# Performance work log

Hardware: AMD Instinct MI355X
Metric: run time of the kernel (lower is better)

The kernel has to match this reference:

```python
import jax, jax.numpy as jnp
import numpy as np

FEATURE_DIM = 512
NUM_HEADS = 8
HEAD_DIM = FEATURE_DIM // NUM_HEADS


def setup_inputs() -> dict:
    key = jax.random.key(0)
    ks = jax.random.split(key, 16)
    B, N, F = 16, 768, FEATURE_DIM
    Nb = N // 3
    s = 1.0 / np.sqrt(F)
    inp = {
        "x_1": jax.random.normal(ks[0], (B, N, F), jnp.float32),
        "x_2": jax.random.normal(ks[1], (B, N, F), jnp.float32),
        "z_b": jax.random.normal(ks[2], (Nb, F), jnp.float32),
        # weights stored [in, out] (torch Linear applies x @ W.T)
        "Wqkv_i": jax.random.normal(ks[3], (F, 3 * F), jnp.float32) * s,
        "Wqkv_j": jax.random.normal(ks[4], (F, 3 * F), jnp.float32) * s,
        "Wqkv_b": jax.random.normal(ks[5], (F, 3 * F), jnp.float32) * s,
        "W_f": jax.random.normal(ks[6], (2 * F, F), jnp.float32) * s,
        "b_f": jnp.zeros((F,), jnp.float32),
        "W_m": jax.random.normal(ks[7], (F, F), jnp.float32) * s,
        "b_m": jnp.zeros((F,), jnp.float32),
        "W_QKV": jax.random.normal(ks[8], (F, 3 * F), jnp.float32) * s,
        "W_proj": jax.random.normal(ks[9], (F, F), jnp.float32) * s,
        "b_proj": jnp.zeros((F,), jnp.float32),
    }
    return inp


def reference(x_1, x_2, z_b, Wqkv_i, Wqkv_j, Wqkv_b, W_f, b_f, W_m, b_m, W_QKV, W_proj, b_proj):
    z_i, z_j = x_1, x_2
    B, N, F = z_i.shape
    Nb = z_b.shape[0]
    scale = F ** -0.5           # full-dim attention scale
    Scale = HEAD_DIM ** -0.5    # multi-head attention scale

    zb = jnp.broadcast_to((z_b * 0.2)[None], (B, Nb, F))

    def split_qkv(x, W):
        qkv = (x @ W).reshape(x.shape[0], x.shape[1], 3, F)
        return qkv[:, :, 0], qkv[:, :, 1], qkv[:, :, 2]

    _, k_i, v_i = split_qkv(z_i, Wqkv_i)
    q_j, _, _ = split_qkv(z_j, Wqkv_j)
    q_b, k_b, v_b = split_qkv(zb, Wqkv_b)

    # bottleneck cross attentions (single-head, full feature dim)
    a_ib = jax.nn.softmax(jnp.einsum('bmf,bnf->bmn', q_b, k_i) * scale, axis=-1)  # [B,Nb,N]
    a_bj = jax.nn.softmax(jnp.einsum('bnf,bmf->bnm', q_j, k_b) * scale, axis=-1)  # [B,N,Nb]

    a_ib = jnp.einsum('bmn,bnf->bmf', a_ib, v_i)  # [B,Nb,F]
    attn_up = jax.nn.softmax(jnp.einsum('bnf,bmf->bnm', z_i, a_ib) * scale, axis=-1)  # [B,N,Nb]
    a_ib = jnp.einsum('bnm,bmf->bnf', attn_up, a_ib)  # [B,N,F]
    a_bj = jnp.einsum('bnm,bmf->bnf', a_bj, v_b)      # [B,N,F]
    a_ij = (a_ib + a_bj) * 0.5

    # gated fusion
    f_ij = jax.nn.sigmoid(jnp.concatenate([a_ij, z_j], axis=-1) @ W_f + b_f)
    h_ij = jax.nn.relu(z_i + (a_ij @ W_m + b_m) * f_ij)

    # standard multi-head self-attention
    QKV = (h_ij @ W_QKV).reshape(B, N, 3, NUM_HEADS, HEAD_DIM)
    Q, K, V = [jnp.transpose(QKV[:, :, t], (0, 2, 1, 3)) for t in range(3)]  # [B,H,N,hd]
    Attn = jax.nn.softmax(jnp.einsum('bhnd,bhmd->bhnm', Q, K) * Scale, axis=-1)
    H = jnp.einsum('bhnm,bhmd->bhnd', Attn, V)
    H = jnp.transpose(H, (0, 2, 1, 3)).reshape(B, N, F)
    return H @ W_proj + b_proj
```

## Files before the change

kernel.cpp:

```cpp
#include <hip/hip_runtime.h>
#include <hip/hip_bf16.h>

typedef __attribute__((ext_vector_type(8))) short short8;
typedef __attribute__((ext_vector_type(4))) float f32x4;
typedef __hip_bfloat16 bf16;
typedef unsigned short ushort;

__device__ __forceinline__ ushort f2b(float v) {
    bf16 h = __float2bfloat16(v);
    return *reinterpret_cast<ushort*>(&h);
}
__device__ __forceinline__ float b2f(ushort u) {
    return __uint_as_float((unsigned)u << 16);
}

#define GLD16(lds, gp) __builtin_amdgcn_global_load_lds( \
    (const __attribute__((address_space(1))) void*)(gp), \
    (__attribute__((address_space(3))) void*)(lds), 16, 0, 0)

template<typename OutT, int EPI, int TM>
__global__ __launch_bounds__(256) void gemm_bf16(
    const bf16* __restrict__ A, const bf16* __restrict__ B, OutT* __restrict__ C,
    int K, int lda, int ldb, int ldc, long sA, long sB, long sC,
    float alpha, const float* __restrict__ bias,
    const float* __restrict__ e1, const float* __restrict__ e2, int eld, long sE,
    bf16* __restrict__ px, bf16* __restrict__ py)
{
    constexpr int RT = TM / 32;
    constexpr int AHW = TM * 32;
    constexpr int BHW = 128 * 32;
    __shared__ __align__(16) bf16 As[2 * AHW];
    __shared__ __align__(16) bf16 Bs[2 * BHW];

    const int t = threadIdx.x;
    const int w = t >> 6, lane = t & 63;
    const int wr = w >> 1, wc = w & 1;
    const int lr = lane & 15, kc4 = lane >> 4;
    const int qr = lane >> 2;
    const int kcr = ((lane & 3) - ((lane >> 3) & 3)) & 3;
    const int row0 = blockIdx.y * TM, col0 = blockIdx.x * 128;
    const int bz = blockIdx.z;

    const bf16* Asel = A; const bf16* Bsel = B;
    int abz = bz; long sBe = sB; int ldbe = ldb;
    if constexpr (EPI == 7) {
        if (bz >= 16) {
            Asel = (const bf16*)px; Bsel = (const bf16*)py;
            abz = bz - 16; sBe = 0; ldbe = eld;
        }
    }
    const bf16* Ab = Asel + (size_t)abz * sA + (size_t)row0 * lda;
    const bf16* Bb = Bsel + (size_t)abz * sBe + (size_t)col0 * ldbe;

    const bf16* ga0; const bf16* ga1 = nullptr;
    if constexpr (TM == 64) {
        ga0 = Ab + (size_t)(w * 16 + qr) * lda + kcr * 8;
    } else {
        ga0 = Ab + (size_t)(w * 32 + qr) * lda + kcr * 8;
        ga1 = Ab + (size_t)(w * 32 + 16 + qr) * lda + kcr * 8;
    }
    const bf16* gb0 = Bb + (size_t)(w * 32 + qr) * ldbe + kcr * 8;
    const bf16* gb1 = Bb + (size_t)(w * 32 + 16 + qr) * ldbe + kcr * 8;
    bf16* lA0; bf16* lA1 = nullptr;
    if constexpr (TM == 64) { lA0 = &As[w * 512]; }
    else                    { lA0 = &As[w * 1024]; lA1 = &As[w * 1024 + 512]; }
    bf16* lB0 = &Bs[w * 1024];
    bf16* lB1 = &Bs[w * 1024 + 512];

    f32x4 acc[RT][4] = {};

    const int cSw = ((kc4 + ((lr >> 1) & 3)) & 3) * 8;
    const bf16* ApBase = &As[(wr * (TM / 2) + lr) * 32 + cSw];
    const bf16* BpBase = &Bs[(wc * 64 + lr) * 32 + cSw];

    GLD16(lA0, ga0);
    if constexpr (TM == 128) GLD16(lA1, ga1);
    GLD16(lB0, gb0); GLD16(lB1, gb1);

    auto step = [&](int kk, int rd, int st) {
        __syncthreads();
        const int kn = kk + 32;
        if (kn < K) {
            GLD16(lA0 + st * AHW, ga0 + kn);
            if constexpr (TM == 128) GLD16(lA1 + st * AHW, ga1 + kn);
            GLD16(lB0 + st * BHW, gb0 + kn);
            GLD16(lB1 + st * BHW, gb1 + kn);
        }
        const bf16* Ap = ApBase + rd * AHW;
        const bf16* Bp = BpBase + rd * BHW;
        short8 af[RT], bfr[4];
#pragma unroll
        for (int i = 0; i < RT; ++i) af[i]  = *(const short8*)(Ap + i * 512);
#pragma unroll
        for (int j = 0; j < 4; ++j) bfr[j] = *(const short8*)(Bp + j * 512);
#pragma unroll
        for (int i = 0; i < RT; ++i)
#pragma unroll
            for (int j = 0; j < 4; ++j)
                acc[i][j] = __builtin_amdgcn_mfma_f32_16x16x32_bf16(af[i], bfr[j], acc[i][j], 0, 0, 0);
    };

    for (int k0 = 0; k0 < K; k0 += 64) {
        step(k0, 0, 1);
        step(k0 + 32, 1, 0);
    }

    if constexpr (EPI == 4) {
        const int sec = blockIdx.x >> 2;
        const int h0 = (blockIdx.x & 3) * 2;
        const int b  = blockIdx.y / 6;
        const int n0 = (blockIdx.y % 6) * TM;
        bf16* dq = (bf16*)C;
#pragma unroll
        for (int j = 0; j < 4; ++j) {
            const int col = wc * 64 + j * 16 + lr;
            const int h = h0 + (col >> 6), hd = col & 63;
            const size_t bh = (size_t)b * 8 + h;
#pragma unroll
            for (int i = 0; i < RT; ++i) {
                const int n = n0 + wr * (TM / 2) + i * 16 + kc4 * 4;
                if (sec == 2) {
                    __align__(8) ushort o[4];
#pragma unroll
                    for (int r = 0; r < 4; ++r) o[r] = f2b(acc[i][j][r]);
                    *(int2*)&py[(bh * 64 + hd) * 768 + n] = *(const int2*)o;
                } else {
                    bf16* d = (sec == 0) ? dq : px;
#pragma unroll
                    for (int r = 0; r < 4; ++r)
                        d[(bh * 768 + n + r) * 64 + hd] = __float2bfloat16(acc[i][j][r]);
                }
            }
        }
        return;
    } else if constexpr (EPI == 5) {
        const int b  = blockIdx.y / 6;
        const int n0 = (blockIdx.y % 6) * TM;
#pragma unroll
        for (int j = 0; j < 4; ++j) {
            const int col = col0 + wc * 64 + j * 16 + lr;
#pragma unroll
            for (int i = 0; i < RT; ++i) {
                const int n = n0 + wr * (TM / 2) + i * 16 + kc4 * 4;
                if (col < 512) {
#pragma unroll
                    for (int r = 0; r < 4; ++r)
                        ((bf16*)C)[((size_t)b * 768 + n + r) * 512 + col] = __float2bfloat16(acc[i][j][r]);
                } else {
                    __align__(8) ushort o[4];
#pragma unroll
                    for (int r = 0; r < 4; ++r) o[r] = f2b(acc[i][j][r]);
                    *(int2*)&py[((size_t)b * 512 + (col - 512)) * 768 + n] = *(const int2*)o;
                }
            }
        }
        return;
    }

    OutT* Cb = C + (size_t)bz * sC;
#pragma unroll
    for (int j = 0; j < 4; ++j) {
        const int col = col0 + wc * 64 + j * 16 + lr;
        const float bv = bias ? bias[col] : 0.f;
#pragma unroll
        for (int i = 0; i < RT; ++i) {
            const int rb = row0 + wr * (TM / 2) + i * 16 + kc4 * 4;
            if constexpr (EPI == 6) {
                __align__(8) ushort o[4];
#pragma unroll
                for (int r = 0; r < 4; ++r) {
                    o[r] = f2b(alpha * acc[i][j][r]);
                    Cb[(size_t)(rb + r) * ldc + col] = __float2bfloat16(alpha * acc[i][j][r]);
                }
                *(int2*)&py[(size_t)bz * sE + (size_t)col * eld + rb] = *(const int2*)o;
            } else {
#pragma unroll
                for (int r = 0; r < 4; ++r) {
                    const int row = rb + r;
                    float v = alpha * acc[i][j][r] + bv;
                    if constexpr (sizeof(OutT) == 2)
                        Cb[(size_t)row * ldc + col] = __float2bfloat16(v);
                    else
                        Cb[(size_t)row * ldc + col] = v;
                }
            }
        }
    }
}

__global__ __launch_bounds__(256) void gemm_gate(
    const bf16* __restrict__ A, const bf16* __restrict__ Bf,
    const bf16* __restrict__ Bm, bf16* __restrict__ Cout,
    const float* __restrict__ bias_f, const float* __restrict__ bias_m,
    const float* __restrict__ x1)
{
    constexpr int AHW = 64 * 32;
    constexpr int BHW = 128 * 32;
    __shared__ __align__(16) bf16 As[2 * AHW];
    __shared__ __align__(16) bf16 FsS[2 * BHW];
    __shared__ __align__(16) bf16 MsS[2 * BHW];

    const int t = threadIdx.x;
    const int w = t >> 6, lane = t & 63;
    const int wr = w >> 1, wc = w & 1;
    const int lr = lane & 15, kc4 = lane >> 4;
    const int qr = lane >> 2;
    const int kcr = ((lane & 3) - ((lane >> 3) & 3)) & 3;
    const int row0 = blockIdx.y * 64, col0 = blockIdx.x * 128;

    const bf16* ga0 = A  + (size_t)(row0 + w * 16 + qr) * 1024 + kcr * 8;
    const bf16* gf0 = Bf + (size_t)(col0 + w * 32 + qr) * 1024 + kcr * 8;
    const bf16* gf1 = Bf + (size_t)(col0 + w * 32 + 16 + qr) * 1024 + kcr * 8;
    const bf16* gm0 = Bm + (size_t)(col0 + w * 32 + qr) * 512 + kcr * 8;
    const bf16* gm1 = Bm + (size_t)(col0 + w * 32 + 16 + qr) * 512 + kcr * 8;
    bf16* lA0 = &As[w * 512];
    bf16* lF0 = &FsS[w * 1024]; bf16* lF1 = &FsS[w * 1024 + 512];
    bf16* lM0 = &MsS[w * 1024]; bf16* lM1 = &MsS[w * 1024 + 512];

    f32x4 acc1[2][4] = {};
    f32x4 acc2[2][4] = {};

    const int cSw = ((kc4 + ((lr >> 1) & 3)) & 3) * 8;
    const bf16* ApBase = &As[(wr * 32 + lr) * 32 + cSw];
    const bf16* FpBase = &FsS[(wc * 64 + lr) * 32 + cSw];
    const bf16* MpBase = &MsS[(wc * 64 + lr) * 32 + cSw];

    GLD16(lA0, ga0);
    GLD16(lF0, gf0); GLD16(lF1, gf1);
    GLD16(lM0, gm0); GLD16(lM1, gm1);

    auto step = [&](int kk, int rd, int st) {
        __syncthreads();
        const int kn = kk + 32;
        if (kn < 1024) {
            GLD16(lA0 + st * AHW, ga0 + kn);
            GLD16(lF0 + st * BHW, gf0 + kn);
            GLD16(lF1 + st * BHW, gf1 + kn);
            if (kn < 512) {
                GLD16(lM0 + st * BHW, gm0 + kn);
                GLD16(lM1 + st * BHW, gm1 + kn);
            }
        }
        const bf16* Ap = ApBase + rd * AHW;
        const bf16* Fp = FpBase + rd * BHW;
        short8 af[2], ff[4];
#pragma unroll
        for (int i = 0; i < 2; ++i) af[i] = *(const short8*)(Ap + i * 512);
#pragma unroll
        for (int j = 0; j < 4; ++j) ff[j] = *(const short8*)(Fp + j * 512);
#pragma unroll
        for (int i = 0; i < 2; ++i)
#pragma unroll
            for (int j = 0; j < 4; ++j)
                acc1[i][j] = __builtin_amdgcn_mfma_f32_16x16x32_bf16(af[i], ff[j], acc1[i][j], 0, 0, 0);
        if (kk < 512) {
            const bf16* Mp = MpBase + rd * BHW;
            short8 mf[4];
#pragma unroll
            for (int j = 0; j < 4; ++j) mf[j] = *(const short8*)(Mp + j * 512);
#pragma unroll
            for (int i = 0; i < 2; ++i)
#pragma unroll
                for (int j = 0; j < 4; ++j)
                    acc2[i][j] = __builtin_amdgcn_mfma_f32_16x16x32_bf16(af[i], mf[j], acc2[i][j], 0, 0, 0);
        }
    };

    for (int k0 = 0; k0 < 1024; k0 += 64) {
        step(k0, 0, 1);
        step(k0 + 32, 1, 0);
    }

#pragma unroll
    for (int j = 0; j < 4; ++j) {
        const int col = col0 + wc * 64 + j * 16 + lr;
        const float bvf = bias_f[col], bvm = bias_m[col];
#pragma unroll
        for (int i = 0; i < 2; ++i) {
            const int rb = row0 + wr * 32 + i * 16 + kc4 * 4;
#pragma unroll
            for (int r = 0; r < 4; ++r) {
                const int row = rb + r;
                const float sig = 1.f / (1.f + __expf(-(acc1[i][j][r] + bvf)));
                const float rr = x1[(size_t)row * 512 + col] + (acc2[i][j][r] + bvm) * sig;
                Cout[(size_t)row * 512 + col] = __float2bfloat16(rr > 0.f ? rr : 0.f);
            }
        }
    }
}

template<typename TI, int NSRC>
__global__ __launch_bounds__(256) void k_transpose(
    const TI* __restrict__ s0, const TI* __restrict__ s1,
    const TI* __restrict__ s2, const TI* __restrict__ s3,
    bf16* __restrict__ dst, int src_ld, int dst_ld, long sSrc, long sDst,
    int rep, long repStride)
{
    __shared__ float tile[64][65];
    const int t = threadIdx.x;
    const int c0 = blockIdx.x * 64, r0 = blockIdx.y * 64;
    const int z = blockIdx.z;
    const TI* src = s0;
    if (NSRC > 1) src = (z == 0) ? s0 : (z == 1) ? s1 : (z == 2) ? s2 : s3;
    {
        const int r = t >> 2, cq = (t & 3) * 16;
        const TI* sp = src + (size_t)z * sSrc + (size_t)(r0 + r) * src_ld + c0 + cq;
        if constexpr (sizeof(TI) == 4) {
#pragma unroll
            for (int u = 0; u < 16; u += 4) {
                float4 v = *(const float4*)((const float*)sp + u);
                tile[r][cq + u]     = v.x; tile[r][cq + u + 1] = v.y;
                tile[r][cq + u + 2] = v.z; tile[r][cq + u + 3] = v.w;
            }
        } else {
            const ushort* up = (const ushort*)sp;
            union { short8 v; ushort u[8]; } p0, p1;
            p0.v = *(const short8*)up; p1.v = *(const short8*)(up + 8);
#pragma unroll
            for (int u = 0; u < 8; ++u) {
                tile[r][cq + u]     = b2f(p0.u[u]);
                tile[r][cq + 8 + u] = b2f(p1.u[u]);
            }
        }
    }
    __syncthreads();
    const int c = t >> 2, rq = (t & 3) * 16;
    __align__(16) ushort ob[16];
#pragma unroll
    for (int u = 0; u < 16; ++u) ob[u] = f2b(tile[rq + u][c]);
    for (int rp = 0; rp < rep; ++rp) {
        bf16* dp = dst + (size_t)rp * repStride + (size_t)z * sDst + (size_t)(c0 + c) * dst_ld + r0 + rq;
        *(int4*)dp       = *(const int4*)&ob[0];
        *(int4*)(dp + 8) = *(const int4*)&ob[8];
    }
}

__global__ __launch_bounds__(256) void k_cast3(const float* __restrict__ x1,
    const float* __restrict__ x2, const float* __restrict__ zb,
    bf16* __restrict__ d1, bf16* __restrict__ d2, bf16* __restrict__ d3)
{
    const int z = blockIdx.z;
    const float* src; bf16* dst; int ld; float scale; int n;
    if (z == 0)      { src = x1; dst = d1; ld = 512;  scale = 1.f;  n = 6291456; }
    else if (z == 1) { src = x2; dst = d2; ld = 1024; scale = 1.f;  n = 6291456; }
    else             { src = zb; dst = d3; ld = 512;  scale = 0.2f; n = 131072;  }
    int i = (blockIdx.x * 256 + threadIdx.x) * 8;
    if (i >= n) return;
    float4 a = *(const float4*)(src + i), b = *(const float4*)(src + i + 4);
    __align__(16) ushort o[8];
    o[0] = f2b(a.x * scale); o[1] = f2b(a.y * scale); o[2] = f2b(a.z * scale); o[3] = f2b(a.w * scale);
    o[4] = f2b(b.x * scale); o[5] = f2b(b.y * scale); o[6] = f2b(b.z * scale); o[7] = f2b(b.w * scale);
    int row = i >> 9, col = i & 511;
    *(int4*)(dst + (size_t)row * ld + col) = *(const int4*)o;
}

template<int COLS, int MODE>
__global__ __launch_bounds__(256) void softmax_wave(const float* __restrict__ X,
                                                    bf16* __restrict__ Y)
{
    const int wv = threadIdx.x >> 6, lane = threadIdx.x & 63;
    const long row = (long)blockIdx.x * 4 + wv;
    const float* src = X + row * COLS;
    constexpr int V = COLS / 64;
    float v[V];
#pragma unroll
    for (int i = 0; i < V; ++i) v[i] = src[lane + i * 64];
    float m = v[0];
#pragma unroll
    for (int i = 1; i < V; ++i) m = fmaxf(m, v[i]);
#pragma unroll
    for (int o = 32; o; o >>= 1) m = fmaxf(m, __shfl_xor(m, o));
    float s = 0.f;
#pragma unroll
    for (int i = 0; i < V; ++i) { v[i] = __expf(v[i] - m); s += v[i]; }
#pragma unroll
    for (int o = 32; o; o >>= 1) s += __shfl_xor(s, o);
    const float inv = 1.f / s;
    bf16* dst;
    if constexpr (MODE == 0) {
        dst = Y + row * COLS;
    } else {
        const int z = (int)(row / 768), mm = (int)(row % 768);
        dst = Y + ((size_t)(z & 15) * 768 + mm) * 512 + (z >> 4) * 256;
    }
#pragma unroll
    for (int i = 0; i < V; ++i) dst[lane + i * 64] = __float2bfloat16(v[i] * inv);
}

__global__ __launch_bounds__(256) void mhsa_flash_mfma(
    const bf16* __restrict__ Qb, const bf16* __restrict__ Kb,
    const bf16* __restrict__ VT, bf16* __restrict__ Hout)
{
    constexpr int LD = 72;
    __shared__ __align__(16) ushort Qs[64 * LD];
    __shared__ __align__(16) ushort Ks[64 * LD];
    __shared__ __align__(16) ushort Vt[64 * LD];
    __shared__ __align__(16) ushort Ps[64 * LD];

    const int t = threadIdx.x;
    const int w = t >> 6, lane = t & 63;
    const int l16 = lane & 15, q4 = lane >> 4;
    const int h = blockIdx.x, b = blockIdx.y, qt = blockIdx.z;
    const size_t bh = (size_t)b * 8 + h;
    const ushort* qbase = (const ushort*)Qb + bh * 768 * 64;
    const ushort* kbase = (const ushort*)Kb + bh * 768 * 64;
    const ushort* vbase = (const ushort*)VT + bh * 64 * 768;

    const int r = t >> 2, c0 = (t & 3) * 16;

    {
        const ushort* src = qbase + (size_t)(qt * 64 + r) * 64 + c0;
        *(int4*)&Qs[r * LD + c0]     = *(const int4*)src;
        *(int4*)&Qs[r * LD + c0 + 8] = *(const int4*)(src + 8);
    }

    int4 ka0, ka1, va0, va1;
    {
        const ushort* ks = kbase + (size_t)r * 64 + c0;
        ka0 = *(const int4*)ks; ka1 = *(const int4*)(ks + 8);
        const ushort* vs = vbase + (size_t)r * 768 + c0;
        va0 = *(const int4*)vs; va1 = *(const int4*)(vs + 8);
    }
    __syncthreads();

    short8 qf0 = *(const short8*)&Qs[(w * 16 + l16) * LD + q4 * 8];
    short8 qf1 = *(const short8*)&Qs[(w * 16 + l16) * LD + 32 + q4 * 8];

    float lsum[4] = {0.f, 0.f, 0.f, 0.f};
    f32x4 acc[4] = {};

    for (int kt = 0; kt < 12; ++kt) {
        if (kt) __syncthreads();
        *(int4*)&Ks[r * LD + c0]     = ka0;
        *(int4*)&Ks[r * LD + c0 + 8] = ka1;
        *(int4*)&Vt[r * LD + c0]     = va0;
        *(int4*)&Vt[r * LD + c0 + 8] = va1;
        __syncthreads();

        if (kt < 11) {
            const ushort* ks = kbase + (size_t)((kt + 1) * 64 + r) * 64 + c0;
            ka0 = *(const int4*)ks; ka1 = *(const int4*)(ks + 8);
            const ushort* vs = vbase + (size_t)r * 768 + (kt + 1) * 64 + c0;
            va0 = *(const int4*)vs; va1 = *(const int4*)(vs + 8);
        }

        f32x4 s[4] = {};
#pragma unroll
        for (int nt = 0; nt < 4; ++nt) {
            short8 kf0 = *(const short8*)&Ks[(nt * 16 + l16) * LD + q4 * 8];
            short8 kf1 = *(const short8*)&Ks[(nt * 16 + l16) * LD + 32 + q4 * 8];
            s[nt] = __builtin_amdgcn_mfma_f32_16x16x32_bf16(qf0, kf0, s[nt], 0, 0, 0);
            s[nt] = __builtin_amdgcn_mfma_f32_16x16x32_bf16(qf1, kf1, s[nt], 0, 0, 0);
        }

#pragma unroll
        for (int nt = 0; nt < 4; ++nt) {
#pragma unroll
            for (int e = 0; e < 4; ++e) {
                const float p = __expf(s[nt][e] * 0.125f);
                lsum[e] += p;
                Ps[(w * 16 + q4 * 4 + e) * LD + nt * 16 + l16] = f2b(p);
            }
        }

        short8 pf0 = *(const short8*)&Ps[(w * 16 + l16) * LD + q4 * 8];
        short8 pf1 = *(const short8*)&Ps[(w * 16 + l16) * LD + 32 + q4 * 8];
#pragma unroll
        for (int jt = 0; jt < 4; ++jt) {
            short8 vf0 = *(const short8*)&Vt[(jt * 16 + l16) * LD + q4 * 8];
            short8 vf1 = *(const short8*)&Vt[(jt * 16 + l16) * LD + 32 + q4 * 8];
            acc[jt] = __builtin_amdgcn_mfma_f32_16x16x32_bf16(pf0, vf0, acc[jt], 0, 0, 0);
            acc[jt] = __builtin_amdgcn_mfma_f32_16x16x32_bf16(pf1, vf1, acc[jt], 0, 0, 0);
        }
    }

    const int orow = qt * 64 + w * 16 + q4 * 4;
#pragma unroll
    for (int e = 0; e < 4; ++e) {
        float l = lsum[e];
        l += __shfl_xor(l, 1);
        l += __shfl_xor(l, 2);
        l += __shfl_xor(l, 4);
        l += __shfl_xor(l, 8);
        const float inv = 1.f / l;
        const size_t rbase = ((size_t)b * 768 + orow + e) * 512 + h * 64;
#pragma unroll
        for (int jt = 0; jt < 4; ++jt)
            Hout[rbase + jt * 16 + l16] = __float2bfloat16(acc[jt][e] * inv);
    }
}

extern "C" void kernel_launch(void* const* d_in, const int* in_sizes, int n_in,
                              void* d_out, int out_size, void* d_ws, size_t ws_size,
                              hipStream_t stream)
{
    (void)in_sizes; (void)n_in; (void)out_size; (void)ws_size;
    const float* x1     = (const float*)d_in[0];
    const float* x2     = (const float*)d_in[1];
    const float* z_b    = (const float*)d_in[2];
    const float* Wqkv_i = (const float*)d_in[3];
    const float* Wqkv_j = (const float*)d_in[4];
    const float* Wqkv_b = (const float*)d_in[5];
    const float* W_f    = (const float*)d_in[6];
    const float* b_f    = (const float*)d_in[7];
    const float* W_m    = (const float*)d_in[8];
    const float* b_m    = (const float*)d_in[9];
    const float* W_QKV  = (const float*)d_in[10];
    const float* W_proj = (const float*)d_in[11];
    const float* b_proj = (const float*)d_in[12];
    float* out = (float*)d_out;

    const float scale = 0.044194173824159216f;

    char* base = (char*)d_ws;
    size_t off = 0;
    auto alloc = [&](size_t bytes) { char* r = base + off; off += (bytes + 255) & ~(size_t)255; return r; };

    char* Rq  = alloc((size_t)3 * 25165824);
    char* R1  = Rq;
    char* R2  = Rq + 25165824;
    char* R3  = Rq + 2 * 25165824;
    char* R4  = alloc(25165824);
    bf16* Wt4     = (bf16*)alloc((size_t)4 * 1536 * 512 * 2);
    bf16* Wt_f    = (bf16*)alloc(512 * 1024 * 2);
    bf16* Wt_mp   = (bf16*)alloc((size_t)2 * 512 * 512 * 2);
    bf16* c_zb    = (bf16*)alloc(256 * 512 * 2);
    bf16* qkvb    = (bf16*)alloc(256 * 1536 * 2);
    bf16* aib0    = (bf16*)alloc((size_t)16 * 256 * 512 * 2);
    bf16* Bcat    = (bf16*)alloc((size_t)16 * 512 * 512 * 2);
    float* S      = (float*)alloc((size_t)32 * 768 * 256 * 4);
    bf16* Sb1     = (bf16*)alloc((size_t)16 * 256 * 768 * 2);
    bf16* Sb_cat  = (bf16*)alloc((size_t)16 * 768 * 512 * 2);
    bf16* c_cat   = (bf16*)alloc((size_t)12288 * 1024 * 2);
    bf16* hbuf    = (bf16*)alloc((size_t)12288 * 512 * 2);

    bf16* Wt_i = Wt4, *Wt_j = Wt4 + 1536 * 512, *Wt_b = Wt4 + 2 * 1536 * 512,
        *Wt_qkv = Wt4 + (size_t)3 * 1536 * 512;
    bf16* Wt_m = Wt_mp, *Wt_proj = Wt_mp + 512 * 512;

    bf16*  Kc   = (bf16*)R1;
    bf16*  Qb   = (bf16*)R1;
    bf16*  Kb   = (bf16*)(R1 + 12582912);
    bf16*  v_iT = (bf16*)R2;
    bf16*  VTb  = (bf16*)R2;
    bf16*  c_x1 = (bf16*)R3;
    bf16*  qj   = (bf16*)R4;   bf16* Hout = (bf16*)R4;

    auto G64 = [&](const bf16* A, const bf16* B, void* C, bool outBf,
                   int M, int N, int K, int lda, int ldb, int ldc,
                   long sA, long sB, long sC, int batch, float alpha, const float* bias) {
        dim3 grid(N / 128, M / 64, batch);
        if (outBf) gemm_bf16<bf16, 0, 64><<<grid, 256, 0, stream>>>(A, B, (bf16*)C, K, lda, ldb, ldc, sA, sB, sC, alpha, bias, nullptr, nullptr, 0, 0, nullptr, nullptr);
        else       gemm_bf16<float, 0, 64><<<grid, 256, 0, stream>>>(A, B, (float*)C, K, lda, ldb, ldc, sA, sB, sC, alpha, bias, nullptr, nullptr, 0, 0, nullptr, nullptr);
    };

    k_cast3<<<dim3(3072, 1, 3), 256, 0, stream>>>(x1, x2, z_b, c_x1, c_cat + 512, c_zb);
    k_transpose<float, 4><<<dim3(24, 8, 4), 256, 0, stream>>>(
        Wqkv_i, Wqkv_j, Wqkv_b, W_QKV, Wt4, 1536, 512, 0, 1536L * 512, 1, 0);
    k_transpose<float, 1><<<dim3(8, 16, 1), 256, 0, stream>>>(
        W_f, nullptr, nullptr, nullptr, Wt_f, 512, 1024, 0, 0, 1, 0);
    k_transpose<float, 2><<<dim3(8, 8, 2), 256, 0, stream>>>(
        W_m, W_proj, nullptr, nullptr, Wt_mp, 512, 512, 0, 512L * 512, 1, 0);

    G64(c_zb, Wt_b, qkvb, true, 256, 1536, 512, 512, 512, 1536, 0, 0, 0, 1, 1.f, nullptr);
    k_transpose<bf16, 1><<<dim3(8, 4, 1), 256, 0, stream>>>(
        qkvb + 1024, nullptr, nullptr, nullptr, Bcat + 256, 1536, 512, 0, 0, 16, 512L * 512);
    gemm_bf16<bf16, 5, 128><<<dim3(8, 96, 1), 256, 0, stream>>>(
        c_x1, Wt_i + 512 * 512, Kc, 512, 512, 512, 512, 0, 0, 0,
        1.f, nullptr, nullptr, nullptr, 0, 0, nullptr, v_iT);
    G64(c_cat + 512, Wt_j, qj, true, 12288, 512, 512, 1024, 512, 512, 0, 0, 0, 1, 1.f, nullptr);
    G64(qkvb, Kc, S, false, 256, 768, 512, 1536, 512, 768, 0, 768L * 512, 256L * 768, 16, scale, nullptr);
    softmax_wave<768, 0><<<1024, 256, 0, stream>>>(S, Sb1);
    gemm_bf16<bf16, 6, 64><<<dim3(4, 4, 16), 256, 0, stream>>>(
        Sb1, v_iT, aib0, 768, 768, 768, 512, 256L * 768, 512L * 768, 256L * 512,
        1.f, nullptr, nullptr, nullptr, 512, 512L * 512, nullptr, Bcat);
    gemm_bf16<float, 7, 64><<<dim3(2, 12, 32), 256, 0, stream>>>(
        c_x1, aib0, S, 512, 512, 512, 256, 768L * 512, 256L * 512, 768L * 256,
        scale, nullptr, nullptr, nullptr, 1536, 0, qj, qkvb + 512);
    softmax_wave<256, 1><<<6144, 256, 0, stream>>>(S, Sb_cat);
    G64(Sb_cat, Bcat, c_cat, true, 768, 512, 512, 512, 512, 1024,
        768L * 512, 512L * 512, 768L * 1024, 16, 0.5f, nullptr);
    gemm_gate<<<dim3(4, 192), 256, 0, stream>>>(c_cat, Wt_f, Wt_m, hbuf, b_f, b_m, x1);
    gemm_bf16<bf16, 4, 128><<<dim3(12, 96, 1), 256, 0, stream>>>(
        hbuf, Wt_qkv, Qb, 512, 512, 512, 0, 0, 0, 0,
        1.f, nullptr, nullptr, nullptr, 0, 0, Kb, VTb);
    mhsa_flash_mfma<<<dim3(8, 16, 12), 256, 0, stream>>>(Qb, Kb, VTb, Hout);
    G64(Hout, Wt_proj, out, false, 12288, 512, 512, 512, 512, 512, 0, 0, 0, 1, 1.f, b_proj);
}
```

Measured before the change: 401.6 us.

## Fold q_j projection into k_b, swizzle GEMM blocks across XCDs, deepen pipeline

Computes q_j·k_b^T as x_2·(Wq_j·k_b^T) by first forming a small G = k_b·Wq_j^T matrix, which removes the 12288x512x512 q_j projection GEMM. The EPI 7 GEMM gains separate lda/stride arguments so it can read x_2 directly from c_cat. Separately, 2D GEMM grids get an XCD-aware block remap for L2 locality. The TM=64 GEMM path now prefetches two 32-wide K planes per barrier, using double the LDS, while the TM=128 path gets a simpler single-plane loop. These bring more LDS use and extra small launches, and change the order of rounding for the bf16 products.

```diff
diff --git a/kernel.cpp b/kernel.cpp
--- a/kernel.cpp
+++ b/kernel.cpp
@@ -17,20 +17,30 @@
 #define GLD16(lds, gp) __builtin_amdgcn_global_load_lds( \
     (const __attribute__((address_space(1))) void*)(gp), \
     (__attribute__((address_space(3))) void*)(lds), 16, 0, 0)
+
+__device__ __forceinline__ void xcd_swizzle(int& bx, int& by) {
+    if (gridDim.z == 1 && (gridDim.y & 7) == 0) {
+        const int id = bx + gridDim.x * by;
+        const int xcd = id & 7, slot = id >> 3;
+        by = xcd * (gridDim.y >> 3) + slot / gridDim.x;
+        bx = slot - (slot / gridDim.x) * gridDim.x;
+    }
+}
 
 template<typename OutT, int EPI, int TM>
 __global__ __launch_bounds__(256) void gemm_bf16(
     const bf16* __restrict__ A, const bf16* __restrict__ B, OutT* __restrict__ C,
     int K, int lda, int ldb, int ldc, long sA, long sB, long sC,
     float alpha, const float* __restrict__ bias,
-    const float* __restrict__ e1, const float* __restrict__ e2, int eld, long sE,
+    int lda2, long sA2, int eld, long sE,
     bf16* __restrict__ px, bf16* __restrict__ py)
 {
     constexpr int RT = TM / 32;
-    constexpr int AHW = TM * 32;
-    constexpr int BHW = 128 * 32;
-    __shared__ __align__(16) bf16 As[2 * AHW];
-    __shared__ __align__(16) bf16 Bs[2 * BHW];
+    constexpr int PLA = TM * 32;
+    constexpr int PLB = 128 * 32;
+    constexpr int NP = (TM == 64) ? 4 : 2;
+    __shared__ __align__(16) bf16 As[NP * PLA];
+    __shared__ __align__(16) bf16 Bs[NP * PLB];
 
     const int t = threadIdx.x;
     const int w = t >> 6, lane = t & 63;
@@ -38,26 +48,28 @@
     const int lr = lane & 15, kc4 = lane >> 4;
     const int qr = lane >> 2;
     const int kcr = ((lane & 3) - ((lane >> 3) & 3)) & 3;
-    const int row0 = blockIdx.y * TM, col0 = blockIdx.x * 128;
+    int bx = blockIdx.x, by = blockIdx.y;
+    xcd_swizzle(bx, by);
+    const int row0 = by * TM, col0 = bx * 128;
     const int bz = blockIdx.z;
 
     const bf16* Asel = A; const bf16* Bsel = B;
-    int abz = bz; long sBe = sB; int ldbe = ldb;
+    int abz = bz; long sBe = sB, sAe = sA; int ldbe = ldb, ldae = lda;
     if constexpr (EPI == 7) {
         if (bz >= 16) {
             Asel = (const bf16*)px; Bsel = (const bf16*)py;
-            abz = bz - 16; sBe = 0; ldbe = eld;
-        }
-    }
-    const bf16* Ab = Asel + (size_t)abz * sA + (size_t)row0 * lda;
+            abz = bz - 16; sBe = 0; ldbe = eld; ldae = lda2; sAe = sA2;
+        }
+    }
+    const bf16* Ab = Asel + (size_t)abz * sAe + (size_t)row0 * ldae;
     const bf16* Bb = Bsel + (size_t)abz * sBe + (size_t)col0 * ldbe;
 
     const bf16* ga0; const bf16* ga1 = nullptr;
     if constexpr (TM == 64) {
-        ga0 = Ab + (size_t)(w * 16 + qr) * lda + kcr * 8;
+        ga0 = Ab + (size_t)(w * 16 + qr) * ldae + kcr * 8;
     } else {
-        ga0 = Ab + (size_t)(w * 32 + qr) * lda + kcr * 8;
-        ga1 = Ab + (size_t)(w * 32 + 16 + qr) * lda + kcr * 8;
+        ga0 = Ab + (size_t)(w * 32 + qr) * ldae + kcr * 8;
+        ga1 = Ab + (size_t)(w * 32 + 16 + qr) * ldae + kcr * 8;
     }
     const bf16* gb0 = Bb + (size_t)(w * 32 + qr) * ldbe + kcr * 8;
     const bf16* gb1 = Bb + (size_t)(w * 32 + 16 + qr) * ldbe + kcr * 8;
@@ -73,21 +85,15 @@
     const bf16* ApBase = &As[(wr * (TM / 2) + lr) * 32 + cSw];
     const bf16* BpBase = &Bs[(wc * 64 + lr) * 32 + cSw];
 
-    GLD16(lA0, ga0);
-    if constexpr (TM == 128) GLD16(lA1, ga1);
-    GLD16(lB0, gb0); GLD16(lB1, gb1);
-
-    auto step = [&](int kk, int rd, int st) {
-        __syncthreads();
-        const int kn = kk + 32;
-        if (kn < K) {
-            GLD16(lA0 + st * AHW, ga0 + kn);
-            if constexpr (TM == 128) GLD16(lA1 + st * AHW, ga1 + kn);
-            GLD16(lB0 + st * BHW, gb0 + kn);
-            GLD16(lB1 + st * BHW, gb1 + kn);
-        }
-        const bf16* Ap = ApBase + rd * AHW;
-        const bf16* Bp = BpBase + rd * BHW;
+    auto stageP = [&](int plane, int ko) {
+        GLD16(lA0 + plane * PLA, ga0 + ko);
+        if constexpr (TM == 128) GLD16(lA1 + plane * PLA, ga1 + ko);
+        GLD16(lB0 + plane * PLB, gb0 + ko);
+        GLD16(lB1 + plane * PLB, gb1 + ko);
+    };
+    auto compP = [&](int plane) {
+        const bf16* Ap = ApBase + plane * PLA;
+        const bf16* Bp = BpBase + plane * PLB;
         short8 af[RT], bfr[4];
 #pragma unroll
         for (int i = 0; i < RT; ++i) af[i]  = *(const short8*)(Ap + i * 512);
@@ -100,16 +106,34 @@
                 acc[i][j] = __builtin_amdgcn_mfma_f32_16x16x32_bf16(af[i], bfr[j], acc[i][j], 0, 0, 0);
     };
 
-    for (int k0 = 0; k0 < K; k0 += 64) {
-        step(k0, 0, 1);
-        step(k0 + 32, 1, 0);
+    if constexpr (TM == 64) {
+        stageP(0, 0); stageP(1, 32);
+        int buf = 0;
+        for (int k0 = 0; k0 < K; k0 += 64) {
+            __syncthreads();
+            if (k0 + 64 < K) {
+                stageP((buf ^ 1) * 2,     k0 + 64);
+                stageP((buf ^ 1) * 2 + 1, k0 + 96);
+            }
+            compP(buf * 2); compP(buf * 2 + 1);
+            buf ^= 1;
+        }
+    } else {
+        stageP(0, 0);
+        int buf = 0;
+        for (int k0 = 0; k0 < K; k0 += 32) {
+            __syncthreads();
+            if (k0 + 32 < K) stageP(buf ^ 1, k0 + 32);
+            compP(buf);
+            buf ^= 1;
+        }
     }
 
     if constexpr (EPI == 4) {
-        const int sec = blockIdx.x >> 2;
-        const int h0 = (blockIdx.x & 3) * 2;
-        const int b  = blockIdx.y / 6;
-        const int n0 = (blockIdx.y % 6) * TM;
+        const int sec = bx >> 2;
+        const int h0 = (bx & 3) * 2;
+        const int b  = by / 6;
+        const int n0 = (by % 6) * TM;
         bf16* dq = (bf16*)C;
 #pragma unroll
         for (int j = 0; j < 4; ++j) {
@@ -134,8 +158,8 @@
         }
         return;
     } else if constexpr (EPI == 5) {
-        const int b  = blockIdx.y / 6;
-        const int n0 = (blockIdx.y % 6) * TM;
+        const int b  = by / 6;
+        const int n0 = (by % 6) * TM;
 #pragma unroll
         for (int j = 0; j < 4; ++j) {
             const int col = col0 + wc * 64 + j * 16 + lr;
@@ -206,7 +230,9 @@
     const int lr = lane & 15, kc4 = lane >> 4;
     const int qr = lane >> 2;
     const int kcr = ((lane & 3) - ((lane >> 3) & 3)) & 3;
-    const int row0 = blockIdx.y * 64, col0 = blockIdx.x * 128;
+    int bx = blockIdx.x, by = blockIdx.y;
+    xcd_swizzle(bx, by);
+    const int row0 = by * 64, col0 = bx * 128;
 
     const bf16* ga0 = A  + (size_t)(row0 + w * 16 + qr) * 1024 + kcr * 8;
     const bf16* gf0 = Bf + (size_t)(col0 + w * 32 + qr) * 1024 + kcr * 8;
@@ -337,16 +363,21 @@
 
 __global__ __launch_bounds__(256) void k_cast3(const float* __restrict__ x1,
     const float* __restrict__ x2, const float* __restrict__ zb,
-    bf16* __restrict__ d1, bf16* __restrict__ d2, bf16* __restrict__ d3)
+    const float* __restrict__ wj,
+    bf16* __restrict__ d1, bf16* __restrict__ d2, bf16* __restrict__ d3,
+    bf16* __restrict__ d4)
 {
     const int z = blockIdx.z;
     const float* src; bf16* dst; int ld; float scale; int n;
     if (z == 0)      { src = x1; dst = d1; ld = 512;  scale = 1.f;  n = 6291456; }
     else if (z == 1) { src = x2; dst = d2; ld = 1024; scale = 1.f;  n = 6291456; }
-    else             { src = zb; dst = d3; ld = 512;  scale = 0.2f; n = 131072;  }
+    else if (z == 2) { src = zb; dst = d3; ld = 512;  scale = 0.2f; n = 131072;  }
+    else             { src = wj; dst = d4; ld = 512;  scale = 1.f;  n = 262144;  }
     int i = (blockIdx.x * 256 + threadIdx.x) * 8;
     if (i >= n) return;
-    float4 a = *(const float4*)(src + i), b = *(const float4*)(src + i + 4);
+    int si = i;
+    if (z == 3) si = (i >> 9) * 1536 + (i & 511);
+    float4 a = *(const float4*)(src + si), b = *(const float4*)(src + si + 4);
     __align__(16) ushort o[8];
     o[0] = f2b(a.x * scale); o[1] = f2b(a.y * scale); o[2] = f2b(a.z * scale); o[3] = f2b(a.w * scale);
     o[4] = f2b(b.x * scale); o[5] = f2b(b.y * scale); o[6] = f2b(b.z * scale); o[7] = f2b(b.w * scale);
@@ -521,9 +552,11 @@
     char* R2  = Rq + 25165824;
     char* R3  = Rq + 2 * 25165824;
     char* R4  = alloc(25165824);
-    bf16* Wt4     = (bf16*)alloc((size_t)4 * 1536 * 512 * 2);
+    bf16* Wt4     = (bf16*)alloc((size_t)3 * 1536 * 512 * 2);
     bf16* Wt_f    = (bf16*)alloc(512 * 1024 * 2);
     bf16* Wt_mp   = (bf16*)alloc((size_t)2 * 512 * 512 * 2);
+    bf16* Wj_bf   = (bf16*)alloc(512 * 512 * 2);
+    bf16* Gbuf    = (bf16*)alloc(256 * 512 * 2);
     bf16* c_zb    = (bf16*)alloc(256 * 512 * 2);
     bf16* qkvb    = (bf16*)alloc(256 * 1536 * 2);
     bf16* aib0    = (bf16*)alloc((size_t)16 * 256 * 512 * 2);
@@ -534,8 +567,8 @@
     bf16* c_cat   = (bf16*)alloc((size_t)12288 * 1024 * 2);
     bf16* hbuf    = (bf16*)alloc((size_t)12288 * 512 * 2);
 
-    bf16* Wt_i = Wt4, *Wt_j = Wt4 + 1536 * 512, *Wt_b = Wt4 + 2 * 1536 * 512,
-        *Wt_qkv = Wt4 + (size_t)3 * 1536 * 512;
+    bf16* Wt_i = Wt4, *Wt_b = Wt4 + 1536 * 512,
+        *Wt_qkv = Wt4 + (size_t)2 * 1536 * 512;
     bf16* Wt_m = Wt_mp, *Wt_proj = Wt_mp + 512 * 512;
 
     bf16*  Kc   = (bf16*)R1;
@@ -544,46 +577,48 @@
     bf16*  v_iT = (bf16*)R2;
     bf16*  VTb  = (bf16*)R2;
     bf16*  c_x1 = (bf16*)R3;
-    bf16*  qj   = (bf16*)R4;   bf16* Hout = (bf16*)R4;
+    bf16*  Hout = (bf16*)R4;
 
     auto G64 = [&](const bf16* A, const bf16* B, void* C, bool outBf,
                    int M, int N, int K, int lda, int ldb, int ldc,
                    long sA, long sB, long sC, int batch, float alpha, const float* bias) {
         dim3 grid(N / 128, M / 64, batch);
-        if (outBf) gemm_bf16<bf16, 0, 64><<<grid, 256, 0, stream>>>(A, B, (bf16*)C, K, lda, ldb, ldc, sA, sB, sC, alpha, bias, nullptr, nullptr, 0, 0, nullptr, nullptr);
-        else       gemm_bf16<float, 0, 64><<<grid, 256, 0, stream>>>(A, B, (float*)C, K, lda, ldb, ldc, sA, sB, sC, alpha, bias, nullptr, nullptr, 0, 0, nullptr, nullptr);
+        if (outBf) gemm_bf16<bf16, 0, 64><<<grid, 256, 0, stream>>>(A, B, (bf16*)C, K, lda, ldb, ldc, sA, sB, sC, alpha, bias, 0, 0, 0, 0, nullptr, nullptr);
+        else       gemm_bf16<float, 0, 64><<<grid, 256, 0, stream>>>(A, B, (float*)C, K, lda, ldb, ldc, sA, sB, sC, alpha, bias, 0, 0, 0, 0, nullptr, nullptr);
     };
 
-    k_cast3<<<dim3(3072, 1, 3), 256, 0, stream>>>(x1, x2, z_b, c_x1, c_cat + 512, c_zb);
-    k_transpose<float, 4><<<dim3(24, 8, 4), 256, 0, stream>>>(
-        Wqkv_i, Wqkv_j, Wqkv_b, W_QKV, Wt4, 1536, 512, 0, 1536L * 512, 1, 0);
+    k_cast3<<<dim3(3072, 1, 4), 256, 0, stream>>>(x1, x2, z_b, Wqkv_j,
+                                                  c_x1, c_cat + 512, c_zb, Wj_bf);
+    k_transpose<float, 3><<<dim3(24, 8, 3), 256, 0, stream>>>(
+        Wqkv_i, Wqkv_b, W_QKV, nullptr, Wt4, 1536, 512, 0, 1536L * 512, 1, 0);
     k_transpose<float, 1><<<dim3(8, 16, 1), 256, 0, stream>>>(
         W_f, nullptr, nullptr, nullptr, Wt_f, 512, 1024, 0, 0, 1, 0);
     k_transpose<float, 2><<<dim3(8, 8, 2), 256, 0, stream>>>(
         W_m, W_proj, nullptr, nullptr, Wt_mp, 512, 512, 0, 512L * 512, 1, 0);
 
     G64(c_zb, Wt_b, qkvb, true, 256, 1536, 512, 512, 512, 1536, 0, 0, 0, 1, 1.f, nullptr);
+    G64(qkvb + 512, Wj_bf, Gbuf, true, 256, 512, 512, 1536, 512, 512, 0, 0, 0, 1, 1.f, nullptr);
     k_transpose<bf16, 1><<<dim3(8, 4, 1), 256, 0, stream>>>(
         qkvb + 1024, nullptr, nullptr, nullptr, Bcat + 256, 1536, 512, 0, 0, 16, 512L * 512);
     gemm_bf16<bf16, 5, 128><<<dim3(8, 96, 1), 256, 0, stream>>>(
         c_x1, Wt_i + 512 * 512, Kc, 512, 512, 512, 512, 0, 0, 0,
-        1.f, nullptr, nullptr, nullptr, 0, 0, nullptr, v_iT);
-    G64(c_cat + 512, Wt_j, qj, true, 12288, 512, 512, 1024, 512, 512, 0, 0, 0, 1, 1.f, nullptr);
+        1.f, nullptr, 0, 0, 0, 0, nullptr, v_iT);
     G64(qkvb, Kc, S, false, 256, 768, 512, 1536, 512, 768, 0, 768L * 512, 256L * 768, 16, scale, nullptr);
     softmax_wave<768, 0><<<1024, 256, 0, stream>>>(S, Sb1);
     gemm_bf16<bf16, 6, 64><<<dim3(4, 4, 16), 256, 0, stream>>>(
         Sb1, v_iT, aib0, 768, 768, 768, 512, 256L * 768, 512L * 768, 256L * 512,
-        1.f, nullptr, nullptr, nullptr, 512, 512L * 512, nullptr, Bcat);
+        1.f, nullptr, 0, 0, 512, 512L * 512, nullptr, Bcat);
     gemm_bf16<float, 7, 64><<<dim3(2, 12, 32), 256, 0, stream>>>(
         c_x1, aib0, S, 512, 512, 512, 256, 768L * 512, 256L * 512, 768L * 256,
-        scale, nullptr, nullptr, nullptr, 1536, 0, qj, qkvb + 512);
+        scale, nullptr, 1024, 768L * 1024, 512, 0,
+        c_cat + 512, Gbuf);
     softmax_wave<256, 1><<<6144, 256, 0, stream>>>(S, Sb_cat);
     G64(Sb_cat, Bcat, c_cat, true, 768, 512, 512, 512, 512, 1024,
         768L * 512, 512L * 512, 768L * 1024, 16, 0.5f, nullptr);
     gemm_gate<<<dim3(4, 192), 256, 0, stream>>>(c_cat, Wt_f, Wt_m, hbuf, b_f, b_m, x1);
     gemm_bf16<bf16, 4, 128><<<dim3(12, 96, 1), 256, 0, stream>>>(
         hbuf, Wt_qkv, Qb, 512, 512, 512, 0, 0, 0, 0,
-        1.f, nullptr, nullptr, nullptr, 0, 0, Kb, VTb);
+        1.f, nullptr, 0, 0, 0, 0, Kb, VTb);
     mhsa_flash_mfma<<<dim3(8, 16, 12), 256, 0, stream>>>(Qb, Kb, VTb, Hout);
     G64(Hout, Wt_proj, out, false, 12288, 512, 512, 512, 512, 512, 0, 0, 0, 1, 1.f, b_proj);
 }
```

Measured after the change: 380.1 us, median of 2. -5.3%, faster.
